# Performance work log

Measured on AMD Instinct MI355X. Metric: run time of the kernel, lower is better.

## Reference

```python
import jax, jax.numpy as jnp
import numpy as np

N, K, W = 500000, 512, 64


def setup_inputs() -> dict:
    key = jax.random.key(0)
    kx, kc = jax.random.split(key)
    X = jax.random.normal(kx, (N, W), dtype=jnp.float32)
    # nn.init.uniform_(codebook.weight, a=-1.0, b=1.0)
    codebook = jax.random.uniform(kc, (K, W), dtype=jnp.float32, minval=-1.0, maxval=1.0)
    return {"X": X, "codebook": codebook}


def reference(X, codebook):
    # torch.cdist (p=2): pairwise Euclidean distances [N, K]
    x2 = jnp.sum(X * X, axis=-1, keepdims=True)          # [N, 1]
    c2 = jnp.sum(codebook * codebook, axis=-1)           # [K]
    d2 = x2 - 2.0 * (X @ codebook.T) + c2[None, :]        # [N, K]
    dist = jnp.sqrt(jnp.maximum(d2, 0.0))
    idx = jnp.argmin(dist, axis=-1)                       # [N] int
    min_dists = jnp.min(dist, axis=-1)                    # [N] == gather(dist, idx)
    return idx, min_dists
```

## Files before the change

kernel.cpp:

```cpp
#include <hip/hip_runtime.h>

#define N_POINTS 500000
#define K_CENT   512
#define W_DIM    64
#define N_SUB    (N_POINTS / 16)
#define N_JOBS   ((N_SUB + 2) / 3)

typedef _Float16 half8 __attribute__((ext_vector_type(8)));
typedef float    f32x4 __attribute__((ext_vector_type(4)));

__global__ void cvt_kernel(const float* __restrict__ cb,
                           _Float16* __restrict__ cbf) {
    int id = blockIdx.x * 256 + threadIdx.x;
    if (id >= K_CENT * 8) return;
    int c = id >> 3, o = (id & 7) * 8;
    int t = c >> 5, csub = (c >> 4) & 1, r = c & 15;
    int kstep = o >> 5, grp = (o >> 3) & 3;
    int lane = grp * 16 + r;
    const float* src = cb + (size_t)c * W_DIM + o;
    half8 h, l;
#pragma unroll
    for (int j = 0; j < 8; ++j) {
        float w = -2.0f * src[j];
        _Float16 hh = (_Float16)w;
        h[j] = hh;
        l[j] = (_Float16)(w - (float)hh);
    }
    size_t bh = ((((size_t)t * 2 + 0) * 2 + csub) * 2 + kstep) * 512 + (size_t)lane * 8;
    size_t bl = ((((size_t)t * 2 + 1) * 2 + csub) * 2 + kstep) * 512 + (size_t)lane * 8;
    *(half8*)(cbf + bh) = h;
    *(half8*)(cbf + bl) = l;
}

__global__ void c2_kernel(const float* __restrict__ cb, float* __restrict__ c2) {
    int c = blockIdx.x * 256 + threadIdx.x;
    if (c >= K_CENT) return;
    const float4* row = (const float4*)(cb + (size_t)c * W_DIM);
    double s = 0.0;
#pragma unroll
    for (int j = 0; j < W_DIM / 4; ++j) {
        float4 v = row[j];
        s += (double)v.x * v.x + (double)v.y * v.y + (double)v.z * v.z + (double)v.w * v.w;
    }
    c2[c] = (float)s;
}

#define MFMA16(A, B, C) __builtin_amdgcn_mfma_f32_16x16x32_f16(A, B, C, 0, 0, 0)

#define PREFETCH_A(T, DH, DL)                                                  \
    {                                                                          \
        const _Float16* nb = cbf + (size_t)(T) * 4096 + (size_t)lane * 8;      \
        DH[0][0] = *(const half8*)(nb + 0 * 512);                              \
        DH[0][1] = *(const half8*)(nb + 1 * 512);                              \
        DH[1][0] = *(const half8*)(nb + 2 * 512);                              \
        DH[1][1] = *(const half8*)(nb + 3 * 512);                              \
        DL[0][0] = *(const half8*)(nb + 2048 + 0 * 512);                       \
        DL[0][1] = *(const half8*)(nb + 2048 + 1 * 512);                       \
        DL[1][0] = *(const half8*)(nb + 2048 + 2 * 512);                       \
        DL[1][1] = *(const half8*)(nb + 2048 + 3 * 512);                       \
    }

#define MFMA_CHUNK(T, AH, AL, NXH, NXL, ACC)                                   \
    {                                                                          \
        int t_ = (T);                                                          \
        if (t_ < 15) { PREFETCH_A(t_ + 1, NXH, NXL) }                          \
        _Pragma("unroll")                                                      \
        for (int cs = 0; cs < 2; ++cs)                                         \
            _Pragma("unroll")                                                  \
            for (int ps = 0; ps < 3; ++ps)                                     \
                ACC[cs][ps] = MFMA16(AH[cs][0], bh[ps][0], cs ? q1 : q0);      \
        _Pragma("unroll")                                                      \
        for (int cs = 0; cs < 2; ++cs)                                         \
            _Pragma("unroll")                                                  \
            for (int ps = 0; ps < 3; ++ps)                                     \
                ACC[cs][ps] = MFMA16(AH[cs][1], bh[ps][1], ACC[cs][ps]);       \
        _Pragma("unroll")                                                      \
        for (int cs = 0; cs < 2; ++cs)                                         \
            _Pragma("unroll")                                                  \
            for (int ps = 0; ps < 3; ++ps)                                     \
                ACC[cs][ps] = MFMA16(AL[cs][0], bh[ps][0], ACC[cs][ps]);       \
        _Pragma("unroll")                                                      \
        for (int cs = 0; cs < 2; ++cs)                                         \
            _Pragma("unroll")                                                  \
            for (int ps = 0; ps < 3; ++ps)                                     \
                ACC[cs][ps] = MFMA16(AL[cs][1], bh[ps][1], ACC[cs][ps]);       \
        _Pragma("unroll")                                                      \
        for (int cs = 0; cs < 2; ++cs)                                         \
            _Pragma("unroll")                                                  \
            for (int ps = 0; ps < 3; ++ps)                                     \
                ACC[cs][ps] = MFMA16(AH[cs][0], bl[ps][0], ACC[cs][ps]);       \
        _Pragma("unroll")                                                      \
        for (int cs = 0; cs < 2; ++cs)                                         \
            _Pragma("unroll")                                                  \
            for (int ps = 0; ps < 3; ++ps)                                     \
                ACC[cs][ps] = MFMA16(AH[cs][1], bl[ps][1], ACC[cs][ps]);       \
        if (t_ < 15) {                                                         \
            q0 = *(const f32x4*)&c2s[(t_ + 1) * 32 + 0 * 16 + grp4];           \
            q1 = *(const f32x4*)&c2s[(t_ + 1) * 32 + 1 * 16 + grp4];           \
        }                                                                      \
    }

#define ARGMIN_CHUNK(T_, ACC)                                                  \
    {                                                                          \
        _Pragma("unroll")                                                      \
        for (int ps = 0; ps < 3; ++ps) {                                       \
            float v0 = ACC[0][ps][0], v1 = ACC[0][ps][1];                      \
            float v2 = ACC[0][ps][2], v3 = ACC[0][ps][3];                      \
            float v4 = ACC[1][ps][0], v5 = ACC[1][ps][1];                      \
            float v6 = ACC[1][ps][2], v7 = ACC[1][ps][3];                      \
            float a0 = fminf(v0, v1), a1 = fminf(v2, v3);                      \
            float a2 = fminf(v4, v5), a3 = fminf(v6, v7);                      \
            float b0 = fminf(a0, a1), b1 = fminf(a2, a3);                      \
            float m  = fminf(b0, b1);                                          \
            bool  L2 = (m == b0);                                              \
            float aL = L2 ? a0 : a2;                                           \
            bool  L1 = (m == aL);                                              \
            float vE = L2 ? (L1 ? v0 : v2) : (L1 ? v4 : v6);                   \
            bool  L0 = (m == vE);                                              \
            int ji = (L2 ? 0 : 4) | (L1 ? 0 : 2) | (L0 ? 0 : 1);               \
            int ci = (T_) * 32 + (ji >> 2) * 16 + grp4 + (ji & 3);             \
            bool imp = m < bd[ps];                                             \
            bd[ps] = imp ? m : bd[ps];                                         \
            bi[ps] = imp ? ci : bi[ps];                                        \
        }                                                                      \
    }

__global__ __launch_bounds__(256, 2)
void kmeans_mfma(const float* __restrict__ X,
                 const _Float16* __restrict__ cbf,
                 const float* __restrict__ c2,
                 float* __restrict__ out_idx,
                 float* __restrict__ out_dist) {
    __shared__ __align__(16) float c2s[K_CENT];
    int tid = threadIdx.x;
    c2s[tid] = c2[tid];
    c2s[tid + 256] = c2[tid + 256];
    __syncthreads();

    int wave = tid >> 6;
    int lane = tid & 63;
    int l15  = lane & 15;
    int grp  = lane >> 4;
    int grp4 = grp * 4;
    int grp8 = grp * 8;

    int job = blockIdx.x * 4 + wave;
    if (job >= N_JOBS) return;
    int sub0 = job * 3;

    half8 bh[3][2], bl[3][2];
    float x2[3] = {0.f, 0.f, 0.f};
#pragma unroll
    for (int ps = 0; ps < 3; ++ps) {
        int p = (sub0 + ps) * 16 + l15;
        int pe = p < N_POINTS ? p : (N_POINTS - 1);
#pragma unroll
        for (int ks = 0; ks < 2; ++ks) {
            const float4* xp = (const float4*)(X + (size_t)pe * W_DIM + ks * 32 + grp8);
            float4 f0 = xp[0], f1 = xp[1];
            float fa[8] = {f0.x, f0.y, f0.z, f0.w, f1.x, f1.y, f1.z, f1.w};
#pragma unroll
            for (int j = 0; j < 8; ++j) {
                _Float16 hh = (_Float16)fa[j];
                bh[ps][ks][j] = hh;
                bl[ps][ks][j] = (_Float16)(fa[j] - (float)hh);
                x2[ps] = fmaf(fa[j], fa[j], x2[ps]);
            }
        }
    }
#pragma unroll
    for (int ps = 0; ps < 3; ++ps) {
        x2[ps] += __shfl_xor(x2[ps], 16);
        x2[ps] += __shfl_xor(x2[ps], 32);
    }

    float bd[3] = {3.4e38f, 3.4e38f, 3.4e38f};
    int   bi[3] = {0, 0, 0};

    f32x4 q0, q1;
    f32x4 accP[2][3], accQ[2][3];
    half8 ahA[2][2], alA[2][2], ahB[2][2], alB[2][2];

    PREFETCH_A(0, ahA, alA)
    q0 = *(const f32x4*)&c2s[0 * 16 + grp4];
    q1 = *(const f32x4*)&c2s[1 * 16 + grp4];

    MFMA_CHUNK(0, ahA, alA, ahB, alB, accP)

#pragma unroll 1
    for (int tt = 0; tt < 7; ++tt) {
        MFMA_CHUNK(2 * tt + 1, ahB, alB, ahA, alA, accQ)
        ARGMIN_CHUNK(2 * tt, accP)
        MFMA_CHUNK(2 * tt + 2, ahA, alA, ahB, alB, accP)
        ARGMIN_CHUNK(2 * tt + 1, accQ)
    }
    MFMA_CHUNK(15, ahB, alB, ahA, alA, accQ)
    ARGMIN_CHUNK(14, accP)
    ARGMIN_CHUNK(15, accQ)

#pragma unroll
    for (int ps = 0; ps < 3; ++ps) {
        float od = __shfl_xor(bd[ps], 16); int oi = __shfl_xor(bi[ps], 16);
        if (od < bd[ps] || (od == bd[ps] && oi < bi[ps])) { bd[ps] = od; bi[ps] = oi; }
        od = __shfl_xor(bd[ps], 32); oi = __shfl_xor(bi[ps], 32);
        if (od < bd[ps] || (od == bd[ps] && oi < bi[ps])) { bd[ps] = od; bi[ps] = oi; }
    }

    if (grp == 0) {
#pragma unroll
        for (int ps = 0; ps < 3; ++ps) {
            int p = (sub0 + ps) * 16 + l15;
            if (p < N_POINTS) {
                out_idx[p]  = (float)bi[ps];
                out_dist[p] = sqrtf(fmaxf(bd[ps] + x2[ps], 0.f));
            }
        }
    }
}

extern "C" void kernel_launch(void* const* d_in, const int* in_sizes, int n_in,
                              void* d_out, int out_size, void* d_ws, size_t ws_size,
                              hipStream_t stream) {
    const float* X  = (const float*)d_in[0];
    const float* cb = (const float*)d_in[1];
    float* out      = (float*)d_out;

    _Float16* cbf = (_Float16*)d_ws;
    float*    c2  = (float*)(cbf + (size_t)K_CENT * W_DIM * 2);

    hipLaunchKernelGGL(cvt_kernel, dim3((K_CENT * 8 + 255) / 256), dim3(256), 0, stream, cb, cbf);
    hipLaunchKernelGGL(c2_kernel, dim3((K_CENT + 255) / 256), dim3(256), 0, stream, cb, c2);

    hipLaunchKernelGGL(kmeans_mfma, dim3((N_JOBS + 3) / 4), dim3(256), 0, stream,
                       X, cbf, c2, out, out + N_POINTS);
}
```

Measured before the change: 104.0 us.

## Stage codebook tiles in LDS via async global_load_lds with block-shared double buffer

Each block now loads every codebook tile once into a double-buffered LDS buffer with direct global-to-LDS loads, split across its four waves. Previously each wave fetched the full codebook through its own registers. Each wave now handles 32 points instead of 48, and the register-level ping-pong of accumulators is replaced by a simple loop with a block barrier per tile. The goal is to cut redundant global/L2 traffic and VGPR pressure, at the price of a __syncthreads per tile, LDS read latency, and less MFMA work per loaded A fragment.

```diff
diff --git a/kernel.cpp b/kernel.cpp
--- a/kernel.cpp
+++ b/kernel.cpp
@@ -3,8 +3,7 @@
 #define N_POINTS 500000
 #define K_CENT   512
 #define W_DIM    64
-#define N_SUB    (N_POINTS / 16)
-#define N_JOBS   ((N_SUB + 2) / 3)
+#define N_JOBS   (N_POINTS / 32)
 
 typedef _Float16 half8 __attribute__((ext_vector_type(8)));
 typedef float    f32x4 __attribute__((ext_vector_type(4)));
@@ -47,83 +46,8 @@
 
 #define MFMA16(A, B, C) __builtin_amdgcn_mfma_f32_16x16x32_f16(A, B, C, 0, 0, 0)
 
-#define PREFETCH_A(T, DH, DL)                                                  \
-    {                                                                          \
-        const _Float16* nb = cbf + (size_t)(T) * 4096 + (size_t)lane * 8;      \
-        DH[0][0] = *(const half8*)(nb + 0 * 512);                              \
-        DH[0][1] = *(const half8*)(nb + 1 * 512);                              \
-        DH[1][0] = *(const half8*)(nb + 2 * 512);                              \
-        DH[1][1] = *(const half8*)(nb + 3 * 512);                              \
-        DL[0][0] = *(const half8*)(nb + 2048 + 0 * 512);                       \
-        DL[0][1] = *(const half8*)(nb + 2048 + 1 * 512);                       \
-        DL[1][0] = *(const half8*)(nb + 2048 + 2 * 512);                       \
-        DL[1][1] = *(const half8*)(nb + 2048 + 3 * 512);                       \
-    }
-
-#define MFMA_CHUNK(T, AH, AL, NXH, NXL, ACC)                                   \
-    {                                                                          \
-        int t_ = (T);                                                          \
-        if (t_ < 15) { PREFETCH_A(t_ + 1, NXH, NXL) }                          \
-        _Pragma("unroll")                                                      \
-        for (int cs = 0; cs < 2; ++cs)                                         \
-            _Pragma("unroll")                                                  \
-            for (int ps = 0; ps < 3; ++ps)                                     \
-                ACC[cs][ps] = MFMA16(AH[cs][0], bh[ps][0], cs ? q1 : q0);      \
-        _Pragma("unroll")                                                      \
-        for (int cs = 0; cs < 2; ++cs)                                         \
-            _Pragma("unroll")                                                  \
-            for (int ps = 0; ps < 3; ++ps)                                     \
-                ACC[cs][ps] = MFMA16(AH[cs][1], bh[ps][1], ACC[cs][ps]);       \
-        _Pragma("unroll")                                                      \
-        for (int cs = 0; cs < 2; ++cs)                                         \
-            _Pragma("unroll")                                                  \
-            for (int ps = 0; ps < 3; ++ps)                                     \
-                ACC[cs][ps] = MFMA16(AL[cs][0], bh[ps][0], ACC[cs][ps]);       \
-        _Pragma("unroll")                                                      \
-        for (int cs = 0; cs < 2; ++cs)                                         \
-            _Pragma("unroll")                                                  \
-            for (int ps = 0; ps < 3; ++ps)                                     \
-                ACC[cs][ps] = MFMA16(AL[cs][1], bh[ps][1], ACC[cs][ps]);       \
-        _Pragma("unroll")                                                      \
-        for (int cs = 0; cs < 2; ++cs)                                         \
-            _Pragma("unroll")                                                  \
-            for (int ps = 0; ps < 3; ++ps)                                     \
-                ACC[cs][ps] = MFMA16(AH[cs][0], bl[ps][0], ACC[cs][ps]);       \
-        _Pragma("unroll")                                                      \
-        for (int cs = 0; cs < 2; ++cs)                                         \
-            _Pragma("unroll")                                                  \
-            for (int ps = 0; ps < 3; ++ps)                                     \
-                ACC[cs][ps] = MFMA16(AH[cs][1], bl[ps][1], ACC[cs][ps]);       \
-        if (t_ < 15) {                                                         \
-            q0 = *(const f32x4*)&c2s[(t_ + 1) * 32 + 0 * 16 + grp4];           \
-            q1 = *(const f32x4*)&c2s[(t_ + 1) * 32 + 1 * 16 + grp4];           \
-        }                                                                      \
-    }
-
-#define ARGMIN_CHUNK(T_, ACC)                                                  \
-    {                                                                          \
-        _Pragma("unroll")                                                      \
-        for (int ps = 0; ps < 3; ++ps) {                                       \
-            float v0 = ACC[0][ps][0], v1 = ACC[0][ps][1];                      \
-            float v2 = ACC[0][ps][2], v3 = ACC[0][ps][3];                      \
-            float v4 = ACC[1][ps][0], v5 = ACC[1][ps][1];                      \
-            float v6 = ACC[1][ps][2], v7 = ACC[1][ps][3];                      \
-            float a0 = fminf(v0, v1), a1 = fminf(v2, v3);                      \
-            float a2 = fminf(v4, v5), a3 = fminf(v6, v7);                      \
-            float b0 = fminf(a0, a1), b1 = fminf(a2, a3);                      \
-            float m  = fminf(b0, b1);                                          \
-            bool  L2 = (m == b0);                                              \
-            float aL = L2 ? a0 : a2;                                           \
-            bool  L1 = (m == aL);                                              \
-            float vE = L2 ? (L1 ? v0 : v2) : (L1 ? v4 : v6);                   \
-            bool  L0 = (m == vE);                                              \
-            int ji = (L2 ? 0 : 4) | (L1 ? 0 : 2) | (L0 ? 0 : 1);               \
-            int ci = (T_) * 32 + (ji >> 2) * 16 + grp4 + (ji & 3);             \
-            bool imp = m < bd[ps];                                             \
-            bd[ps] = imp ? m : bd[ps];                                         \
-            bi[ps] = imp ? ci : bi[ps];                                        \
-        }                                                                      \
-    }
+typedef __attribute__((address_space(3))) _Float16 lds_f16;
+typedef __attribute__((address_space(1))) const _Float16 glb_f16;
 
 __global__ __launch_bounds__(256, 2)
 void kmeans_mfma(const float* __restrict__ X,
@@ -131,11 +55,11 @@
                  const float* __restrict__ c2,
                  float* __restrict__ out_idx,
                  float* __restrict__ out_dist) {
-    __shared__ __align__(16) float c2s[K_CENT];
+    __shared__ _Float16 abuf[2][4096];
+    __shared__ float c2s[K_CENT];
     int tid = threadIdx.x;
     c2s[tid] = c2[tid];
     c2s[tid + 256] = c2[tid + 256];
-    __syncthreads();
 
     int wave = tid >> 6;
     int lane = tid & 63;
@@ -144,19 +68,18 @@
     int grp4 = grp * 4;
     int grp8 = grp * 8;
 
-    int job = blockIdx.x * 4 + wave;
-    if (job >= N_JOBS) return;
-    int sub0 = job * 3;
-
-    half8 bh[3][2], bl[3][2];
-    float x2[3] = {0.f, 0.f, 0.f};
-#pragma unroll
-    for (int ps = 0; ps < 3; ++ps) {
-        int p = (sub0 + ps) * 16 + l15;
-        int pe = p < N_POINTS ? p : (N_POINTS - 1);
+    int job   = blockIdx.x * 4 + wave;
+    int valid = job < N_JOBS;
+    int jc    = valid ? job : (N_JOBS - 1);
+
+    half8 bh[2][2], bl[2][2];
+    float x2[2] = {0.f, 0.f};
+#pragma unroll
+    for (int ps = 0; ps < 2; ++ps) {
+        int p = jc * 32 + ps * 16 + l15;
 #pragma unroll
         for (int ks = 0; ks < 2; ++ks) {
-            const float4* xp = (const float4*)(X + (size_t)pe * W_DIM + ks * 32 + grp8);
+            const float4* xp = (const float4*)(X + (size_t)p * W_DIM + ks * 32 + grp8);
             float4 f0 = xp[0], f1 = xp[1];
             float fa[8] = {f0.x, f0.y, f0.z, f0.w, f1.x, f1.y, f1.z, f1.w};
 #pragma unroll
@@ -169,51 +92,114 @@
         }
     }
 #pragma unroll
-    for (int ps = 0; ps < 3; ++ps) {
+    for (int ps = 0; ps < 2; ++ps) {
         x2[ps] += __shfl_xor(x2[ps], 16);
         x2[ps] += __shfl_xor(x2[ps], 32);
     }
 
-    float bd[3] = {3.4e38f, 3.4e38f, 3.4e38f};
-    int   bi[3] = {0, 0, 0};
-
-    f32x4 q0, q1;
-    f32x4 accP[2][3], accQ[2][3];
-    half8 ahA[2][2], alA[2][2], ahB[2][2], alB[2][2];
-
-    PREFETCH_A(0, ahA, alA)
-    q0 = *(const f32x4*)&c2s[0 * 16 + grp4];
-    q1 = *(const f32x4*)&c2s[1 * 16 + grp4];
-
-    MFMA_CHUNK(0, ahA, alA, ahB, alB, accP)
+    float bd[2] = {3.4e38f, 3.4e38f};
+    int   bi[2] = {0, 0};
+
+    {
+        glb_f16* g = (glb_f16*)(cbf + (size_t)wave * 1024 + (size_t)lane * 8);
+        __builtin_amdgcn_global_load_lds((const __attribute__((address_space(1))) void*)g,
+                                         (__attribute__((address_space(3))) void*)&abuf[0][wave * 1024], 16, 0, 0);
+        __builtin_amdgcn_global_load_lds((const __attribute__((address_space(1))) void*)(g + 512),
+                                         (__attribute__((address_space(3))) void*)&abuf[0][wave * 1024 + 512], 16, 0, 0);
+    }
+    __syncthreads();
 
 #pragma unroll 1
-    for (int tt = 0; tt < 7; ++tt) {
-        MFMA_CHUNK(2 * tt + 1, ahB, alB, ahA, alA, accQ)
-        ARGMIN_CHUNK(2 * tt, accP)
-        MFMA_CHUNK(2 * tt + 2, ahA, alA, ahB, alB, accP)
-        ARGMIN_CHUNK(2 * tt + 1, accQ)
-    }
-    MFMA_CHUNK(15, ahB, alB, ahA, alA, accQ)
-    ARGMIN_CHUNK(14, accP)
-    ARGMIN_CHUNK(15, accQ)
-
-#pragma unroll
-    for (int ps = 0; ps < 3; ++ps) {
+    for (int t = 0; t < 16; ++t) {
+        int b = t & 1;
+        if (t < 15) {
+            glb_f16* g = (glb_f16*)(cbf + (size_t)(t + 1) * 4096 + (size_t)wave * 1024 + (size_t)lane * 8);
+            __builtin_amdgcn_global_load_lds((const __attribute__((address_space(1))) void*)g,
+                                             (__attribute__((address_space(3))) void*)&abuf[b ^ 1][wave * 1024], 16, 0, 0);
+            __builtin_amdgcn_global_load_lds((const __attribute__((address_space(1))) void*)(g + 512),
+                                             (__attribute__((address_space(3))) void*)&abuf[b ^ 1][wave * 1024 + 512], 16, 0, 0);
+        }
+        half8 aH[2][2], aL[2][2];
+#pragma unroll
+        for (int cs = 0; cs < 2; ++cs)
+#pragma unroll
+            for (int ks = 0; ks < 2; ++ks) {
+                aH[cs][ks] = *(const half8*)&abuf[b][(0 * 4 + cs * 2 + ks) * 512 + lane * 8];
+                aL[cs][ks] = *(const half8*)&abuf[b][(1 * 4 + cs * 2 + ks) * 512 + lane * 8];
+            }
+        f32x4 q0 = *(const f32x4*)&c2s[t * 32 + grp4];
+        f32x4 q1 = *(const f32x4*)&c2s[t * 32 + 16 + grp4];
+
+        f32x4 acc[2][2];
+#pragma unroll
+        for (int cs = 0; cs < 2; ++cs)
+#pragma unroll
+            for (int ps = 0; ps < 2; ++ps)
+                acc[cs][ps] = MFMA16(aH[cs][0], bh[ps][0], cs ? q1 : q0);
+#pragma unroll
+        for (int cs = 0; cs < 2; ++cs)
+#pragma unroll
+            for (int ps = 0; ps < 2; ++ps)
+                acc[cs][ps] = MFMA16(aH[cs][1], bh[ps][1], acc[cs][ps]);
+#pragma unroll
+        for (int cs = 0; cs < 2; ++cs)
+#pragma unroll
+            for (int ps = 0; ps < 2; ++ps)
+                acc[cs][ps] = MFMA16(aL[cs][0], bh[ps][0], acc[cs][ps]);
+#pragma unroll
+        for (int cs = 0; cs < 2; ++cs)
+#pragma unroll
+            for (int ps = 0; ps < 2; ++ps)
+                acc[cs][ps] = MFMA16(aL[cs][1], bh[ps][1], acc[cs][ps]);
+#pragma unroll
+        for (int cs = 0; cs < 2; ++cs)
+#pragma unroll
+            for (int ps = 0; ps < 2; ++ps)
+                acc[cs][ps] = MFMA16(aH[cs][0], bl[ps][0], acc[cs][ps]);
+#pragma unroll
+        for (int cs = 0; cs < 2; ++cs)
+#pragma unroll
+            for (int ps = 0; ps < 2; ++ps)
+                acc[cs][ps] = MFMA16(aH[cs][1], bl[ps][1], acc[cs][ps]);
+
+#pragma unroll
+        for (int ps = 0; ps < 2; ++ps) {
+            float v0 = acc[0][ps][0], v1 = acc[0][ps][1];
+            float v2 = acc[0][ps][2], v3 = acc[0][ps][3];
+            float v4 = acc[1][ps][0], v5 = acc[1][ps][1];
+            float v6 = acc[1][ps][2], v7 = acc[1][ps][3];
+            float a0 = fminf(v0, v1), a1 = fminf(v2, v3);
+            float a2 = fminf(v4, v5), a3 = fminf(v6, v7);
+            float b0 = fminf(a0, a1), b1 = fminf(a2, a3);
+            float m  = fminf(b0, b1);
+            bool  L2 = (m == b0);
+            float aL2 = L2 ? a0 : a2;
+            bool  L1 = (m == aL2);
+            float vE = L2 ? (L1 ? v0 : v2) : (L1 ? v4 : v6);
+            bool  L0 = (m == vE);
+            int ji = (L2 ? 0 : 4) | (L1 ? 0 : 2) | (L0 ? 0 : 1);
+            int ci = t * 32 + (ji >> 2) * 16 + grp4 + (ji & 3);
+            bool imp = m < bd[ps];
+            bd[ps] = imp ? m : bd[ps];
+            bi[ps] = imp ? ci : bi[ps];
+        }
+        __syncthreads();
+    }
+
+#pragma unroll
+    for (int ps = 0; ps < 2; ++ps) {
         float od = __shfl_xor(bd[ps], 16); int oi = __shfl_xor(bi[ps], 16);
         if (od < bd[ps] || (od == bd[ps] && oi < bi[ps])) { bd[ps] = od; bi[ps] = oi; }
         od = __shfl_xor(bd[ps], 32); oi = __shfl_xor(bi[ps], 32);
         if (od < bd[ps] || (od == bd[ps] && oi < bi[ps])) { bd[ps] = od; bi[ps] = oi; }
     }
 
-    if (grp == 0) {
-#pragma unroll
-        for (int ps = 0; ps < 3; ++ps) {
-            int p = (sub0 + ps) * 16 + l15;
-            if (p < N_POINTS) {
-                out_idx[p]  = (float)bi[ps];
-                out_dist[p] = sqrtf(fmaxf(bd[ps] + x2[ps], 0.f));
-            }
+    if (valid && grp == 0) {
+#pragma unroll
+        for (int ps = 0; ps < 2; ++ps) {
+            int p = jc * 32 + ps * 16 + l15;
+            out_idx[p]  = (float)bi[ps];
+            out_dist[p] = sqrtf(fmaxf(bd[ps] + x2[ps], 0.f));
         }
     }
 }
```

Measured after the change: 104.4 us. No clear change (+0.4%).

## Stage codebook tiles in LDS via async global_load_lds shared across waves

Applied to the files above, without the earlier changes.

Instead of each wave loading its own copy of the fp16 codebook tiles from global memory into registers, the block now cooperatively stages each 32-centroid tile into a double-buffered LDS array using global_load_lds. All four waves then read the tile from LDS. Each wave now processes 32 points instead of 48, and per-block tile rotation is added to spread global reads. MFMA sections are raised in priority with s_setprio, and the argmin merges two tiles per step with index tie-breaking. This cuts redundant global/L2 traffic and register pressure, at the cost of block-wide barriers and less work per wave.

```diff
diff --git a/kernel.cpp b/kernel.cpp
--- a/kernel.cpp
+++ b/kernel.cpp
@@ -3,8 +3,7 @@
 #define N_POINTS 500000
 #define K_CENT   512
 #define W_DIM    64
-#define N_SUB    (N_POINTS / 16)
-#define N_JOBS   ((N_SUB + 2) / 3)
+#define N_JOBS   (N_POINTS / 32)
 
 typedef _Float16 half8 __attribute__((ext_vector_type(8)));
 typedef float    f32x4 __attribute__((ext_vector_type(4)));
@@ -47,79 +46,97 @@
 
 #define MFMA16(A, B, C) __builtin_amdgcn_mfma_f32_16x16x32_f16(A, B, C, 0, 0, 0)
 
-#define PREFETCH_A(T, DH, DL)                                                  \
+#define STAGE(T, BUF)                                                          \
     {                                                                          \
-        const _Float16* nb = cbf + (size_t)(T) * 4096 + (size_t)lane * 8;      \
-        DH[0][0] = *(const half8*)(nb + 0 * 512);                              \
-        DH[0][1] = *(const half8*)(nb + 1 * 512);                              \
-        DH[1][0] = *(const half8*)(nb + 2 * 512);                              \
-        DH[1][1] = *(const half8*)(nb + 3 * 512);                              \
-        DL[0][0] = *(const half8*)(nb + 2048 + 0 * 512);                       \
-        DL[0][1] = *(const half8*)(nb + 2048 + 1 * 512);                       \
-        DL[1][0] = *(const half8*)(nb + 2048 + 2 * 512);                       \
-        DL[1][1] = *(const half8*)(nb + 2048 + 3 * 512);                       \
-    }
-
-#define MFMA_CHUNK(T, AH, AL, NXH, NXL, ACC)                                   \
+        const __attribute__((address_space(1))) _Float16* g =                  \
+            (const __attribute__((address_space(1))) _Float16*)                \
+            (cbf + (size_t)(T) * 4096 + (size_t)wave * 1024 + (size_t)lane * 8); \
+        __builtin_amdgcn_global_load_lds(                                      \
+            (const __attribute__((address_space(1))) void*)g,                  \
+            (__attribute__((address_space(3))) void*)&abuf[BUF][wave * 1024],  \
+            16, 0, 0);                                                         \
+        __builtin_amdgcn_global_load_lds(                                      \
+            (const __attribute__((address_space(1))) void*)(g + 512),          \
+            (__attribute__((address_space(3))) void*)&abuf[BUF][wave * 1024 + 512], \
+            16, 0, 0);                                                         \
+    }
+
+#define MFMA_PHASE(BUF, ACC, Q0, Q1)                                           \
     {                                                                          \
-        int t_ = (T);                                                          \
-        if (t_ < 15) { PREFETCH_A(t_ + 1, NXH, NXL) }                          \
-        _Pragma("unroll")                                                      \
-        for (int cs = 0; cs < 2; ++cs)                                         \
-            _Pragma("unroll")                                                  \
-            for (int ps = 0; ps < 3; ++ps)                                     \
-                ACC[cs][ps] = MFMA16(AH[cs][0], bh[ps][0], cs ? q1 : q0);      \
-        _Pragma("unroll")                                                      \
-        for (int cs = 0; cs < 2; ++cs)                                         \
-            _Pragma("unroll")                                                  \
-            for (int ps = 0; ps < 3; ++ps)                                     \
-                ACC[cs][ps] = MFMA16(AH[cs][1], bh[ps][1], ACC[cs][ps]);       \
-        _Pragma("unroll")                                                      \
-        for (int cs = 0; cs < 2; ++cs)                                         \
-            _Pragma("unroll")                                                  \
-            for (int ps = 0; ps < 3; ++ps)                                     \
-                ACC[cs][ps] = MFMA16(AL[cs][0], bh[ps][0], ACC[cs][ps]);       \
-        _Pragma("unroll")                                                      \
-        for (int cs = 0; cs < 2; ++cs)                                         \
-            _Pragma("unroll")                                                  \
-            for (int ps = 0; ps < 3; ++ps)                                     \
-                ACC[cs][ps] = MFMA16(AL[cs][1], bh[ps][1], ACC[cs][ps]);       \
-        _Pragma("unroll")                                                      \
-        for (int cs = 0; cs < 2; ++cs)                                         \
-            _Pragma("unroll")                                                  \
-            for (int ps = 0; ps < 3; ++ps)                                     \
-                ACC[cs][ps] = MFMA16(AH[cs][0], bl[ps][0], ACC[cs][ps]);       \
-        _Pragma("unroll")                                                      \
-        for (int cs = 0; cs < 2; ++cs)                                         \
-            _Pragma("unroll")                                                  \
-            for (int ps = 0; ps < 3; ++ps)                                     \
-                ACC[cs][ps] = MFMA16(AH[cs][1], bl[ps][1], ACC[cs][ps]);       \
-        if (t_ < 15) {                                                         \
-            q0 = *(const f32x4*)&c2s[(t_ + 1) * 32 + 0 * 16 + grp4];           \
-            q1 = *(const f32x4*)&c2s[(t_ + 1) * 32 + 1 * 16 + grp4];           \
-        }                                                                      \
-    }
-
-#define ARGMIN_CHUNK(T_, ACC)                                                  \
+        half8 aH[2][2], aL[2][2];                                              \
+        _Pragma("unroll")                                                      \
+        for (int cs = 0; cs < 2; ++cs)                                         \
+            _Pragma("unroll")                                                  \
+            for (int ks = 0; ks < 2; ++ks) {                                   \
+                aH[cs][ks] = *(const half8*)&abuf[BUF][(cs * 2 + ks) * 512 + lane * 8]; \
+                aL[cs][ks] = *(const half8*)&abuf[BUF][(4 + cs * 2 + ks) * 512 + lane * 8]; \
+            }                                                                  \
+        __builtin_amdgcn_s_setprio(1);                                         \
+        _Pragma("unroll")                                                      \
+        for (int cs = 0; cs < 2; ++cs)                                         \
+            _Pragma("unroll")                                                  \
+            for (int ps = 0; ps < 2; ++ps)                                     \
+                ACC[cs][ps] = MFMA16(aH[cs][0], bh[ps][0], cs ? Q1 : Q0);      \
+        _Pragma("unroll")                                                      \
+        for (int cs = 0; cs < 2; ++cs)                                         \
+            _Pragma("unroll")                                                  \
+            for (int ps = 0; ps < 2; ++ps)                                     \
+                ACC[cs][ps] = MFMA16(aH[cs][1], bh[ps][1], ACC[cs][ps]);       \
+        _Pragma("unroll")                                                      \
+        for (int cs = 0; cs < 2; ++cs)                                         \
+            _Pragma("unroll")                                                  \
+            for (int ps = 0; ps < 2; ++ps)                                     \
+                ACC[cs][ps] = MFMA16(aL[cs][0], bh[ps][0], ACC[cs][ps]);       \
+        _Pragma("unroll")                                                      \
+        for (int cs = 0; cs < 2; ++cs)                                         \
+            _Pragma("unroll")                                                  \
+            for (int ps = 0; ps < 2; ++ps)                                     \
+                ACC[cs][ps] = MFMA16(aL[cs][1], bh[ps][1], ACC[cs][ps]);       \
+        _Pragma("unroll")                                                      \
+        for (int cs = 0; cs < 2; ++cs)                                         \
+            _Pragma("unroll")                                                  \
+            for (int ps = 0; ps < 2; ++ps)                                     \
+                ACC[cs][ps] = MFMA16(aH[cs][0], bl[ps][0], ACC[cs][ps]);       \
+        _Pragma("unroll")                                                      \
+        for (int cs = 0; cs < 2; ++cs)                                         \
+            _Pragma("unroll")                                                  \
+            for (int ps = 0; ps < 2; ++ps)                                     \
+                ACC[cs][ps] = MFMA16(aH[cs][1], bl[ps][1], ACC[cs][ps]);       \
+        __builtin_amdgcn_s_setprio(0);                                         \
+    }
+
+#define PAIR_ARGMIN(TA)                                                        \
     {                                                                          \
         _Pragma("unroll")                                                      \
-        for (int ps = 0; ps < 3; ++ps) {                                       \
-            float v0 = ACC[0][ps][0], v1 = ACC[0][ps][1];                      \
-            float v2 = ACC[0][ps][2], v3 = ACC[0][ps][3];                      \
-            float v4 = ACC[1][ps][0], v5 = ACC[1][ps][1];                      \
-            float v6 = ACC[1][ps][2], v7 = ACC[1][ps][3];                      \
-            float a0 = fminf(v0, v1), a1 = fminf(v2, v3);                      \
-            float a2 = fminf(v4, v5), a3 = fminf(v6, v7);                      \
+        for (int ps = 0; ps < 2; ++ps) {                                       \
+            float v0 = accP[0][ps][0], v1 = accP[0][ps][1];                    \
+            float v2 = accP[0][ps][2], v3 = accP[0][ps][3];                    \
+            float v4 = accP[1][ps][0], v5 = accP[1][ps][1];                    \
+            float v6 = accP[1][ps][2], v7 = accP[1][ps][3];                    \
+            float v8 = accQ[0][ps][0], v9 = accQ[0][ps][1];                    \
+            float v10 = accQ[0][ps][2], v11 = accQ[0][ps][3];                  \
+            float v12 = accQ[1][ps][0], v13 = accQ[1][ps][1];                  \
+            float v14 = accQ[1][ps][2], v15 = accQ[1][ps][3];                  \
+            float a0 = fminf(v0, v1),   a1 = fminf(v2, v3);                    \
+            float a2 = fminf(v4, v5),   a3 = fminf(v6, v7);                    \
+            float a4 = fminf(v8, v9),   a5 = fminf(v10, v11);                  \
+            float a6 = fminf(v12, v13), a7 = fminf(v14, v15);                  \
             float b0 = fminf(a0, a1), b1 = fminf(a2, a3);                      \
-            float m  = fminf(b0, b1);                                          \
-            bool  L2 = (m == b0);                                              \
-            float aL = L2 ? a0 : a2;                                           \
+            float b2 = fminf(a4, a5), b3 = fminf(a6, a7);                      \
+            float c0 = fminf(b0, b1), c1 = fminf(b2, b3);                      \
+            float m  = fminf(c0, c1);                                          \
+            bool  L3 = (m == c0);                                              \
+            float bL = L3 ? b0 : b2;                                           \
+            bool  L2 = (m == bL);                                              \
+            float aL = L3 ? (L2 ? a0 : a2) : (L2 ? a4 : a6);                   \
             bool  L1 = (m == aL);                                              \
-            float vE = L2 ? (L1 ? v0 : v2) : (L1 ? v4 : v6);                   \
+            float vE = L3 ? (L2 ? (L1 ? v0 : v2) : (L1 ? v4 : v6))             \
+                          : (L2 ? (L1 ? v8 : v10) : (L1 ? v12 : v14));         \
             bool  L0 = (m == vE);                                              \
-            int ji = (L2 ? 0 : 4) | (L1 ? 0 : 2) | (L0 ? 0 : 1);               \
-            int ci = (T_) * 32 + (ji >> 2) * 16 + grp4 + (ji & 3);             \
-            bool imp = m < bd[ps];                                             \
+            int ji = (L3 ? 0 : 8) | (L2 ? 0 : 4) | (L1 ? 0 : 2) | (L0 ? 0 : 1); \
+            int jj = ji & 7;                                                   \
+            int ci = ((TA) + (ji >> 3)) * 32 + (jj >> 2) * 16 + grp4 + (jj & 3); \
+            bool imp = (m < bd[ps]) || (m == bd[ps] && ci < bi[ps]);           \
             bd[ps] = imp ? m : bd[ps];                                         \
             bi[ps] = imp ? ci : bi[ps];                                        \
         }                                                                      \
@@ -131,11 +148,11 @@
                  const float* __restrict__ c2,
                  float* __restrict__ out_idx,
                  float* __restrict__ out_dist) {
-    __shared__ __align__(16) float c2s[K_CENT];
+    __shared__ _Float16 abuf[2][4096];
+    __shared__ float c2s[K_CENT];
     int tid = threadIdx.x;
     c2s[tid] = c2[tid];
     c2s[tid + 256] = c2[tid + 256];
-    __syncthreads();
 
     int wave = tid >> 6;
     int lane = tid & 63;
@@ -143,20 +160,20 @@
     int grp  = lane >> 4;
     int grp4 = grp * 4;
     int grp8 = grp * 8;
-
-    int job = blockIdx.x * 4 + wave;
-    if (job >= N_JOBS) return;
-    int sub0 = job * 3;
-
-    half8 bh[3][2], bl[3][2];
-    float x2[3] = {0.f, 0.f, 0.f};
-#pragma unroll
-    for (int ps = 0; ps < 3; ++ps) {
-        int p = (sub0 + ps) * 16 + l15;
-        int pe = p < N_POINTS ? p : (N_POINTS - 1);
+    int rot  = (blockIdx.x & 7) * 2;
+
+    int job   = blockIdx.x * 4 + wave;
+    int valid = job < N_JOBS;
+    int jc    = valid ? job : (N_JOBS - 1);
+
+    half8 bh[2][2], bl[2][2];
+    float x2[2] = {0.f, 0.f};
+#pragma unroll
+    for (int ps = 0; ps < 2; ++ps) {
+        int p = jc * 32 + ps * 16 + l15;
 #pragma unroll
         for (int ks = 0; ks < 2; ++ks) {
-            const float4* xp = (const float4*)(X + (size_t)pe * W_DIM + ks * 32 + grp8);
+            const float4* xp = (const float4*)(X + (size_t)p * W_DIM + ks * 32 + grp8);
             float4 f0 = xp[0], f1 = xp[1];
             float fa[8] = {f0.x, f0.y, f0.z, f0.w, f1.x, f1.y, f1.z, f1.w};
 #pragma unroll
@@ -169,51 +186,51 @@
         }
     }
 #pragma unroll
-    for (int ps = 0; ps < 3; ++ps) {
+    for (int ps = 0; ps < 2; ++ps) {
         x2[ps] += __shfl_xor(x2[ps], 16);
         x2[ps] += __shfl_xor(x2[ps], 32);
     }
 
-    float bd[3] = {3.4e38f, 3.4e38f, 3.4e38f};
-    int   bi[3] = {0, 0, 0};
-
-    f32x4 q0, q1;
-    f32x4 accP[2][3], accQ[2][3];
-    half8 ahA[2][2], alA[2][2], ahB[2][2], alB[2][2];
-
-    PREFETCH_A(0, ahA, alA)
-    q0 = *(const f32x4*)&c2s[0 * 16 + grp4];
-    q1 = *(const f32x4*)&c2s[1 * 16 + grp4];
-
-    MFMA_CHUNK(0, ahA, alA, ahB, alB, accP)
+    float bd[2] = {3.4e38f, 3.4e38f};
+    int   bi[2] = {0, 0};
+    f32x4 accP[2][2], accQ[2][2];
+
+    STAGE(rot, 0)
+    __syncthreads();
 
 #pragma unroll 1
-    for (int tt = 0; tt < 7; ++tt) {
-        MFMA_CHUNK(2 * tt + 1, ahB, alB, ahA, alA, accQ)
-        ARGMIN_CHUNK(2 * tt, accP)
-        MFMA_CHUNK(2 * tt + 2, ahA, alA, ahB, alB, accP)
-        ARGMIN_CHUNK(2 * tt + 1, accQ)
-    }
-    MFMA_CHUNK(15, ahB, alB, ahA, alA, accQ)
-    ARGMIN_CHUNK(14, accP)
-    ARGMIN_CHUNK(15, accQ)
-
-#pragma unroll
-    for (int ps = 0; ps < 3; ++ps) {
+    for (int it = 0; it < 8; ++it) {
+        int ta = (rot + 2 * it) & 15;
+        f32x4 qa0 = *(const f32x4*)&c2s[ta * 32 + grp4];
+        f32x4 qa1 = *(const f32x4*)&c2s[ta * 32 + 16 + grp4];
+        f32x4 qb0 = *(const f32x4*)&c2s[ta * 32 + 32 + grp4];
+        f32x4 qb1 = *(const f32x4*)&c2s[ta * 32 + 48 + grp4];
+        STAGE(ta + 1, 1)
+        MFMA_PHASE(0, accP, qa0, qa1)
+        __syncthreads();
+        if (it < 7) {
+            int tn = (ta + 2) & 15;
+            STAGE(tn, 0)
+        }
+        MFMA_PHASE(1, accQ, qb0, qb1)
+        PAIR_ARGMIN(ta)
+        __syncthreads();
+    }
+
+#pragma unroll
+    for (int ps = 0; ps < 2; ++ps) {
         float od = __shfl_xor(bd[ps], 16); int oi = __shfl_xor(bi[ps], 16);
         if (od < bd[ps] || (od == bd[ps] && oi < bi[ps])) { bd[ps] = od; bi[ps] = oi; }
         od = __shfl_xor(bd[ps], 32); oi = __shfl_xor(bi[ps], 32);
         if (od < bd[ps] || (od == bd[ps] && oi < bi[ps])) { bd[ps] = od; bi[ps] = oi; }
     }
 
-    if (grp == 0) {
-#pragma unroll
-        for (int ps = 0; ps < 3; ++ps) {
-            int p = (sub0 + ps) * 16 + l15;
-            if (p < N_POINTS) {
-                out_idx[p]  = (float)bi[ps];
-                out_dist[p] = sqrtf(fmaxf(bd[ps] + x2[ps], 0.f));
-            }
+    if (valid && grp == 0) {
+#pragma unroll
+        for (int ps = 0; ps < 2; ++ps) {
+            int p = jc * 32 + ps * 16 + l15;
+            out_idx[p]  = (float)bi[ps];
+            out_dist[p] = sqrtf(fmaxf(bd[ps] + x2[ps], 0.f));
         }
     }
 }
```

Result: faster. 101.5 us (-2.4%).
